# Performance work log

Measured on AMD Instinct MI355X. Metric: run time of the kernel, lower is better.

Reference implementation:

```python
import jax, jax.numpy as jnp
import numpy as np

TEMPERATURE = 0.5
EPS = 1e-8  # torch F.cosine_similarity norm clamp


def setup_inputs() -> dict:
    key = jax.random.key(0)
    k1, k2 = jax.random.split(key)
    B, D = 4096, 512
    return {
        "features_1": jax.random.normal(k1, (B, D), dtype=jnp.float32),
        "features_2": jax.random.normal(k2, (B, D), dtype=jnp.float32),
    }


def reference(features_1, features_2):
    B = features_1.shape[0]
    z = jnp.concatenate([features_1, features_2], axis=0)  # [2B, D]
    norm = jnp.maximum(jnp.linalg.norm(z, axis=1, keepdims=True), EPS)
    zn = z / norm
    # pairwise cosine similarity via single GEMM instead of (2B,2B,D) broadcast
    logits = (zn @ zn.T) / TEMPERATURE  # [2B, 2B]
    labels = jnp.concatenate([jnp.arange(B), jnp.arange(B)])  # [2B]
    logp = jax.nn.log_softmax(logits, axis=1)
    loss = -jnp.mean(logp[jnp.arange(2 * B), labels])
    return loss
```

## Files before the change

kernel.cpp:

```cpp
#include <hip/hip_runtime.h>
#include <hip/hip_bf16.h>

#define B_ROWS 4096
#define N2 8192
#define DD 512
#define NBLK 544

typedef __attribute__((ext_vector_type(4))) float float4v;
typedef __attribute__((ext_vector_type(2))) long long2v;

__global__ __launch_bounds__(256) void k_norm_tgt(const float* __restrict__ f1,
                                                  const float* __restrict__ f2,
                                                  unsigned char* __restrict__ zn8,
                                                  float* __restrict__ tpart,
                                                  float* __restrict__ rowsum) {
  int w = threadIdx.x >> 6, lane = threadIdx.x & 63;
  int j = blockIdx.x * 4 + w;
  const float4* s1 = (const float4*)(f1 + (size_t)j * DD);
  const float4* s2 = (const float4*)(f2 + (size_t)j * DD);
  float4 a0 = s1[lane * 2], a1 = s1[lane * 2 + 1];
  float4 b0 = s2[lane * 2], b1 = s2[lane * 2 + 1];
  float ss1 = a0.x * a0.x + a0.y * a0.y + a0.z * a0.z + a0.w * a0.w +
              a1.x * a1.x + a1.y * a1.y + a1.z * a1.z + a1.w * a1.w;
  float ss2 = b0.x * b0.x + b0.y * b0.y + b0.z * b0.z + b0.w * b0.w +
              b1.x * b1.x + b1.y * b1.y + b1.z * b1.z + b1.w * b1.w;
  float ab = a0.x * b0.x + a0.y * b0.y + a0.z * b0.z + a0.w * b0.w +
             a1.x * b1.x + a1.y * b1.y + a1.z * b1.z + a1.w * b1.w;
#pragma unroll
  for (int o = 1; o < 64; o <<= 1) {
    ss1 += __shfl_xor(ss1, o, 64);
    ss2 += __shfl_xor(ss2, o, 64);
    ab += __shfl_xor(ab, o, 64);
  }
  float inv1 = 1.0f / fmaxf(sqrtf(ss1), 1e-8f);
  float inv2 = 1.0f / fmaxf(sqrtf(ss2), 1e-8f);

  uint2 q;
  int lo = __builtin_amdgcn_cvt_pk_fp8_f32(a0.x * inv1, a0.y * inv1, 0, false);
  lo = __builtin_amdgcn_cvt_pk_fp8_f32(a0.z * inv1, a0.w * inv1, lo, true);
  q.x = (unsigned int)lo;
  lo = __builtin_amdgcn_cvt_pk_fp8_f32(a1.x * inv1, a1.y * inv1, 0, false);
  lo = __builtin_amdgcn_cvt_pk_fp8_f32(a1.z * inv1, a1.w * inv1, lo, true);
  q.y = (unsigned int)lo;
  ((uint2*)(zn8 + (size_t)j * DD))[lane] = q;

  lo = __builtin_amdgcn_cvt_pk_fp8_f32(b0.x * inv2, b0.y * inv2, 0, false);
  lo = __builtin_amdgcn_cvt_pk_fp8_f32(b0.z * inv2, b0.w * inv2, lo, true);
  q.x = (unsigned int)lo;
  lo = __builtin_amdgcn_cvt_pk_fp8_f32(b1.x * inv2, b1.y * inv2, 0, false);
  lo = __builtin_amdgcn_cvt_pk_fp8_f32(b1.z * inv2, b1.w * inv2, lo, true);
  q.y = (unsigned int)lo;
  ((uint2*)(zn8 + (size_t)(B_ROWS + j) * DD))[lane] = q;

  if (lane == 0) tpart[j] = 2.0f + 2.0f * ab * inv1 * inv2;
  if (threadIdx.x < 8) rowsum[blockIdx.x * 8 + threadIdx.x] = 0.f;
}

__global__ __launch_bounds__(256, 4) void k_gemm_expsum(const unsigned char* __restrict__ zn8,
                                                        float* __restrict__ rowsum) {
  __shared__ __align__(16) char bbuf[32768];
  __shared__ float colaccum[512];

  int g = blockIdx.x;

  int P = 0, off = 0;
  for (;;) {
    int nb = (128 - 2 * P + 7) >> 3;
    if (g < off + nb) break;
    off += nb;
    ++P;
  }
  int c = g - off;
  int j0 = 2 * P + 8 * c;
  int nt = 128 - j0; if (nt > 8) nt = 8;
  const int jmir0 = 2 * P + 2;

  const int tid = threadIdx.x;
  const int lane = tid & 63, w = tid >> 6;
  const int lr = lane & 15, hi2 = lane >> 4;
  const char* zb = (const char*)zn8;
  const int arow0 = P * 128;

  colaccum[tid] = 0.f;
  colaccum[tid + 256] = 0.f;

  int srow[8], scol[8];
#pragma unroll
  for (int cc = 0; cc < 8; ++cc) {
    int lo2 = cc * 4096 + tid * 16;
    srow[cc] = lo2 >> 9;
    scol[cc] = (lo2 & 511) ^ ((srow[cc] & 7) << 4);
  }

#define STAGE(rowbase) do {                                                              \
    _Pragma("unroll")                                                                    \
    for (int cc = 0; cc < 8; ++cc) {                                                     \
      const char* _s = zb + (size_t)((rowbase) + srow[cc]) * DD + scol[cc];              \
      __builtin_amdgcn_global_load_lds((__attribute__((address_space(1))) void*)_s,      \
          (__attribute__((address_space(3))) void*)(bbuf + cc * 4096 + tid * 16 - lane * 16), \
          16, 0, 0);                                                                     \
    }                                                                                    \
  } while (0)

  long2v aR[2][8];
  STAGE(arow0);
  __syncthreads();
  if (w < 2) {
#pragma unroll
    for (int m = 0; m < 2; ++m) {
      int rr = (w << 5) + (m << 4) + lr;
      const char* rowp = bbuf + rr * DD;
      int sz = (rr & 7) << 4;
#pragma unroll
      for (int p = 0; p < 8; ++p)
        aR[m][p] = *(const long2v*)(rowp + ((p * 64 + hi2 * 16) ^ sz));
    }
  }
  __syncthreads();
  STAGE(arow0 + 64);
  __syncthreads();
  if (w >= 2) {
#pragma unroll
    for (int m = 0; m < 2; ++m) {
      int rr = ((w - 2) << 5) + (m << 4) + lr;
      const char* rowp = bbuf + rr * DD;
      int sz = (rr & 7) << 4;
#pragma unroll
      for (int p = 0; p < 8; ++p)
        aR[m][p] = *(const long2v*)(rowp + ((p * 64 + hi2 * 16) ^ sz));
    }
  }
  __syncthreads();

  float rowacc[2][4];
#pragma unroll
  for (int m = 0; m < 2; ++m)
#pragma unroll
    for (int r = 0; r < 4; ++r) rowacc[m][r] = 0.f;

  const float Cc = 2.88539008177792681f;
  for (int t = 0; t < nt; ++t) {
    STAGE((j0 + t) * 64);
    __syncthreads();

    float4v acc[2][4];
#pragma unroll
    for (int m = 0; m < 2; ++m)
#pragma unroll
      for (int n = 0; n < 4; ++n) acc[m][n] = {0.f, 0.f, 0.f, 0.f};

#pragma unroll
    for (int n = 0; n < 4; ++n) {
      long2v bR[8];
      int col = (n << 4) + lr;
      const char* colp = bbuf + col * DD;
      int sz = (col & 7) << 4;
#pragma unroll
      for (int p = 0; p < 8; ++p)
        bR[p] = *(const long2v*)(colp + ((p * 64 + hi2 * 16) ^ sz));
#pragma unroll
      for (int p = 0; p < 8; ++p)
#pragma unroll
        for (int m = 0; m < 2; ++m) {
          acc[m][n] = __builtin_amdgcn_mfma_f32_16x16x32_fp8_fp8(aR[m][p][0], bR[p][0], acc[m][n], 0, 0, 0);
          acc[m][n] = __builtin_amdgcn_mfma_f32_16x16x32_fp8_fp8(aR[m][p][1], bR[p][1], acc[m][n], 0, 0, 0);
        }
    }

    float colp4[4] = {0.f, 0.f, 0.f, 0.f};
#pragma unroll
    for (int m = 0; m < 2; ++m)
#pragma unroll
      for (int n = 0; n < 4; ++n)
#pragma unroll
        for (int r = 0; r < 4; ++r) {
          float e = exp2f(fmaf(acc[m][n][r], Cc, -Cc));
          rowacc[m][r] += e;
          colp4[n] += e;
        }
    if ((j0 + t) >= jmir0) {
#pragma unroll
      for (int n = 0; n < 4; ++n) {
        float v = colp4[n];
        v += __shfl_xor(v, 16);
        v += __shfl_xor(v, 32);
        if (hi2 == 0) atomicAdd(&colaccum[(t << 6) + (n << 4) + lr], v);
      }
    }
    __syncthreads();
  }
#undef STAGE

#pragma unroll
  for (int m = 0; m < 2; ++m)
#pragma unroll
    for (int r = 0; r < 4; ++r) {
      float v = rowacc[m][r];
      v += __shfl_xor(v, 1);
      v += __shfl_xor(v, 2);
      v += __shfl_xor(v, 4);
      v += __shfl_xor(v, 8);
      if (lr == 0)
        atomicAdd(&rowsum[arow0 + (w << 5) + (m << 4) + (hi2 << 2) + r], v);
    }
  for (int idx = tid; idx < nt * 64; idx += 256) {
    float v = colaccum[idx];
    if (v != 0.f) atomicAdd(&rowsum[(j0 + (idx >> 6)) * 64 + (idx & 63)], v);
  }
}

__global__ __launch_bounds__(1024) void k_finalize(const float* __restrict__ rowsum,
                                                   const float* __restrict__ tpart,
                                                   float* __restrict__ out) {
  int t = threadIdx.x;
  float acc = 0.f;
  for (int i = t; i < N2; i += 1024) acc += 2.0f + logf(rowsum[i]);
  for (int i = t; i < B_ROWS; i += 1024) acc -= tpart[i];
#pragma unroll
  for (int o = 32; o; o >>= 1) acc += __shfl_down(acc, o, 64);
  __shared__ float wsum[16];
  if ((t & 63) == 0) wsum[t >> 6] = acc;
  __syncthreads();
  if (t == 0) {
    float s = 0.f;
#pragma unroll
    for (int k = 0; k < 16; ++k) s += wsum[k];
    out[0] = s * (1.0f / (float)N2);
  }
}

extern "C" void kernel_launch(void* const* d_in, const int* in_sizes, int n_in,
                              void* d_out, int out_size, void* d_ws, size_t ws_size,
                              hipStream_t stream) {
  const float* f1 = (const float*)d_in[0];
  const float* f2 = (const float*)d_in[1];
  float* out = (float*)d_out;
  char* ws = (char*)d_ws;

  unsigned char* zn8 = (unsigned char*)ws;
  float* rowsum = (float*)(ws + (size_t)N2 * DD);
  float* tpart = rowsum + N2;

  k_norm_tgt<<<B_ROWS / 4, 256, 0, stream>>>(f1, f2, zn8, tpart, rowsum);
  k_gemm_expsum<<<NBLK, 256, 0, stream>>>(zn8, rowsum);
  k_finalize<<<1, 1024, 0, stream>>>(rowsum, tpart, out);
}
```

Measured before the change: 70.10 us.

## Shrink GEMM row tile from 128 to 64 rows and double block count

Each block in the symmetric GEMM+exp-sum kernel now covers a 64-row A panel instead of 128, and each wave holds one 16-row fragment instead of two. The triangular tile schedule is recomputed for 64-row panels, so the grid doubles to 1088 blocks. This is meant to spread work more evenly across CUs and lower per-thread register use. In exchange, every B tile is reused by half as many A rows, so LDS staging traffic and column atomics roughly double. The column-sum flush also drops its zero check and skips the diagonal tile by index instead.

```diff
diff --git a/kernel.cpp b/kernel.cpp
--- a/kernel.cpp
+++ b/kernel.cpp
@@ -4,7 +4,7 @@
 #define B_ROWS 4096
 #define N2 8192
 #define DD 512
-#define NBLK 544
+#define NBLK 1088
 
 typedef __attribute__((ext_vector_type(4))) float float4v;
 typedef __attribute__((ext_vector_type(2))) long long2v;
@@ -65,21 +65,20 @@
 
   int P = 0, off = 0;
   for (;;) {
-    int nb = (128 - 2 * P + 7) >> 3;
+    int nb = (128 - P + 7) >> 3;
     if (g < off + nb) break;
     off += nb;
     ++P;
   }
   int c = g - off;
-  int j0 = 2 * P + 8 * c;
+  int j0 = P + 8 * c;
   int nt = 128 - j0; if (nt > 8) nt = 8;
-  const int jmir0 = 2 * P + 2;
 
   const int tid = threadIdx.x;
   const int lane = tid & 63, w = tid >> 6;
   const int lr = lane & 15, hi2 = lane >> 4;
   const char* zb = (const char*)zn8;
-  const int arow0 = P * 128;
+  const int arow0 = P * 64;
 
   colaccum[tid] = 0.f;
   colaccum[tid + 256] = 0.f;
@@ -97,57 +96,34 @@
     for (int cc = 0; cc < 8; ++cc) {                                                     \
       const char* _s = zb + (size_t)((rowbase) + srow[cc]) * DD + scol[cc];              \
       __builtin_amdgcn_global_load_lds((__attribute__((address_space(1))) void*)_s,      \
-          (__attribute__((address_space(3))) void*)(bbuf + cc * 4096 + tid * 16 - lane * 16), \
+          (__attribute__((address_space(3))) void*)(bbuf + cc * 4096 + (w << 10)),       \
           16, 0, 0);                                                                     \
     }                                                                                    \
   } while (0)
 
-  long2v aR[2][8];
+  long2v aR[8];
   STAGE(arow0);
   __syncthreads();
-  if (w < 2) {
-#pragma unroll
-    for (int m = 0; m < 2; ++m) {
-      int rr = (w << 5) + (m << 4) + lr;
-      const char* rowp = bbuf + rr * DD;
-      int sz = (rr & 7) << 4;
-#pragma unroll
-      for (int p = 0; p < 8; ++p)
-        aR[m][p] = *(const long2v*)(rowp + ((p * 64 + hi2 * 16) ^ sz));
-    }
+  {
+    int rr = (w << 4) + lr;
+    const char* rowp = bbuf + rr * DD;
+    int sz = (rr & 7) << 4;
+#pragma unroll
+    for (int p = 0; p < 8; ++p)
+      aR[p] = *(const long2v*)(rowp + ((p * 64 + hi2 * 16) ^ sz));
   }
   __syncthreads();
-  STAGE(arow0 + 64);
-  __syncthreads();
-  if (w >= 2) {
-#pragma unroll
-    for (int m = 0; m < 2; ++m) {
-      int rr = ((w - 2) << 5) + (m << 4) + lr;
-      const char* rowp = bbuf + rr * DD;
-      int sz = (rr & 7) << 4;
-#pragma unroll
-      for (int p = 0; p < 8; ++p)
-        aR[m][p] = *(const long2v*)(rowp + ((p * 64 + hi2 * 16) ^ sz));
-    }
-  }
-  __syncthreads();
-
-  float rowacc[2][4];
-#pragma unroll
-  for (int m = 0; m < 2; ++m)
-#pragma unroll
-    for (int r = 0; r < 4; ++r) rowacc[m][r] = 0.f;
-
+
+  float rowacc[4] = {0.f, 0.f, 0.f, 0.f};
   const float Cc = 2.88539008177792681f;
+
   for (int t = 0; t < nt; ++t) {
     STAGE((j0 + t) * 64);
     __syncthreads();
 
-    float4v acc[2][4];
-#pragma unroll
-    for (int m = 0; m < 2; ++m)
-#pragma unroll
-      for (int n = 0; n < 4; ++n) acc[m][n] = {0.f, 0.f, 0.f, 0.f};
+    float4v acc[4];
+#pragma unroll
+    for (int n = 0; n < 4; ++n) acc[n] = {0.f, 0.f, 0.f, 0.f};
 
 #pragma unroll
     for (int n = 0; n < 4; ++n) {
@@ -159,26 +135,22 @@
       for (int p = 0; p < 8; ++p)
         bR[p] = *(const long2v*)(colp + ((p * 64 + hi2 * 16) ^ sz));
 #pragma unroll
-      for (int p = 0; p < 8; ++p)
-#pragma unroll
-        for (int m = 0; m < 2; ++m) {
-          acc[m][n] = __builtin_amdgcn_mfma_f32_16x16x32_fp8_fp8(aR[m][p][0], bR[p][0], acc[m][n], 0, 0, 0);
-          acc[m][n] = __builtin_amdgcn_mfma_f32_16x16x32_fp8_fp8(aR[m][p][1], bR[p][1], acc[m][n], 0, 0, 0);
-        }
+      for (int p = 0; p < 8; ++p) {
+        acc[n] = __builtin_amdgcn_mfma_f32_16x16x32_fp8_fp8(aR[p][0], bR[p][0], acc[n], 0, 0, 0);
+        acc[n] = __builtin_amdgcn_mfma_f32_16x16x32_fp8_fp8(aR[p][1], bR[p][1], acc[n], 0, 0, 0);
+      }
     }
 
     float colp4[4] = {0.f, 0.f, 0.f, 0.f};
 #pragma unroll
-    for (int m = 0; m < 2; ++m)
-#pragma unroll
-      for (int n = 0; n < 4; ++n)
-#pragma unroll
-        for (int r = 0; r < 4; ++r) {
-          float e = exp2f(fmaf(acc[m][n][r], Cc, -Cc));
-          rowacc[m][r] += e;
-          colp4[n] += e;
-        }
-    if ((j0 + t) >= jmir0) {
+    for (int n = 0; n < 4; ++n)
+#pragma unroll
+      for (int r = 0; r < 4; ++r) {
+        float e = exp2f(fmaf(acc[n][r], Cc, -Cc));
+        rowacc[r] += e;
+        colp4[n] += e;
+      }
+    if ((j0 + t) > P) {
 #pragma unroll
       for (int n = 0; n < 4; ++n) {
         float v = colp4[n];
@@ -192,21 +164,17 @@
 #undef STAGE
 
 #pragma unroll
-  for (int m = 0; m < 2; ++m)
-#pragma unroll
-    for (int r = 0; r < 4; ++r) {
-      float v = rowacc[m][r];
-      v += __shfl_xor(v, 1);
-      v += __shfl_xor(v, 2);
-      v += __shfl_xor(v, 4);
-      v += __shfl_xor(v, 8);
-      if (lr == 0)
-        atomicAdd(&rowsum[arow0 + (w << 5) + (m << 4) + (hi2 << 2) + r], v);
-    }
-  for (int idx = tid; idx < nt * 64; idx += 256) {
-    float v = colaccum[idx];
-    if (v != 0.f) atomicAdd(&rowsum[(j0 + (idx >> 6)) * 64 + (idx & 63)], v);
-  }
+  for (int r = 0; r < 4; ++r) {
+    float v = rowacc[r];
+    v += __shfl_xor(v, 1);
+    v += __shfl_xor(v, 2);
+    v += __shfl_xor(v, 4);
+    v += __shfl_xor(v, 8);
+    if (lr == 0)
+      atomicAdd(&rowsum[arow0 + (w << 4) + (hi2 << 2) + r], v);
+  }
+  for (int idx = tid + (c == 0 ? 64 : 0); idx < nt * 64; idx += 256)
+    atomicAdd(&rowsum[(j0 + (idx >> 6)) * 64 + (idx & 63)], colaccum[idx]);
 }
 
 __global__ __launch_bounds__(1024) void k_finalize(const float* __restrict__ rowsum,
```

Measured after the change: 69.56 us. About the same (-0.8%).

## Load GEMM operands directly from global memory and halve tiles per block

Applied to the files above, without the earlier changes.

Removes the LDS staging buffer and its per-tile barriers, so the fp8 A and B fragments are read straight from global memory (L2) into registers. It also halves the number of column tiles per block from 8 to 4, roughly doubling the grid. The occupancy hint drops to 3 waves per SIMD. Removing the barriers and LDS traffic is meant to increase overlap, at the cost of uncoalesced 16-byte global reads per lane and more redundant A-tile loads across blocks.

```diff
diff --git a/kernel.cpp b/kernel.cpp
--- a/kernel.cpp
+++ b/kernel.cpp
@@ -4,7 +4,7 @@
 #define B_ROWS 4096
 #define N2 8192
 #define DD 512
-#define NBLK 544
+#define NBLK 1056
 
 typedef __attribute__((ext_vector_type(4))) float float4v;
 typedef __attribute__((ext_vector_type(2))) long long2v;
@@ -56,24 +56,22 @@
   if (threadIdx.x < 8) rowsum[blockIdx.x * 8 + threadIdx.x] = 0.f;
 }
 
-__global__ __launch_bounds__(256, 4) void k_gemm_expsum(const unsigned char* __restrict__ zn8,
+__global__ __launch_bounds__(256, 3) void k_gemm_expsum(const unsigned char* __restrict__ zn8,
                                                         float* __restrict__ rowsum) {
-  __shared__ __align__(16) char bbuf[32768];
-  __shared__ float colaccum[512];
+  __shared__ float colaccum[256];
 
   int g = blockIdx.x;
 
   int P = 0, off = 0;
   for (;;) {
-    int nb = (128 - 2 * P + 7) >> 3;
+    int nb = (131 - 2 * P) >> 2;
     if (g < off + nb) break;
     off += nb;
     ++P;
   }
   int c = g - off;
-  int j0 = 2 * P + 8 * c;
-  int nt = 128 - j0; if (nt > 8) nt = 8;
-  const int jmir0 = 2 * P + 2;
+  const int j0 = 2 * P + 4 * c;
+  int nt = 128 - j0; if (nt > 4) nt = 4;
 
   const int tid = threadIdx.x;
   const int lane = tid & 63, w = tid >> 6;
@@ -81,56 +79,17 @@
   const char* zb = (const char*)zn8;
   const int arow0 = P * 128;
 
-  colaccum[tid] = 0.f;
-  colaccum[tid + 256] = 0.f;
-
-  int srow[8], scol[8];
-#pragma unroll
-  for (int cc = 0; cc < 8; ++cc) {
-    int lo2 = cc * 4096 + tid * 16;
-    srow[cc] = lo2 >> 9;
-    scol[cc] = (lo2 & 511) ^ ((srow[cc] & 7) << 4);
-  }
-
-#define STAGE(rowbase) do {                                                              \
-    _Pragma("unroll")                                                                    \
-    for (int cc = 0; cc < 8; ++cc) {                                                     \
-      const char* _s = zb + (size_t)((rowbase) + srow[cc]) * DD + scol[cc];              \
-      __builtin_amdgcn_global_load_lds((__attribute__((address_space(1))) void*)_s,      \
-          (__attribute__((address_space(3))) void*)(bbuf + cc * 4096 + tid * 16 - lane * 16), \
-          16, 0, 0);                                                                     \
-    }                                                                                    \
-  } while (0)
+  if (tid < 256) colaccum[tid] = 0.f;
+  __syncthreads();
 
   long2v aR[2][8];
-  STAGE(arow0);
-  __syncthreads();
-  if (w < 2) {
-#pragma unroll
-    for (int m = 0; m < 2; ++m) {
-      int rr = (w << 5) + (m << 4) + lr;
-      const char* rowp = bbuf + rr * DD;
-      int sz = (rr & 7) << 4;
-#pragma unroll
-      for (int p = 0; p < 8; ++p)
-        aR[m][p] = *(const long2v*)(rowp + ((p * 64 + hi2 * 16) ^ sz));
-    }
-  }
-  __syncthreads();
-  STAGE(arow0 + 64);
-  __syncthreads();
-  if (w >= 2) {
-#pragma unroll
-    for (int m = 0; m < 2; ++m) {
-      int rr = ((w - 2) << 5) + (m << 4) + lr;
-      const char* rowp = bbuf + rr * DD;
-      int sz = (rr & 7) << 4;
-#pragma unroll
-      for (int p = 0; p < 8; ++p)
-        aR[m][p] = *(const long2v*)(rowp + ((p * 64 + hi2 * 16) ^ sz));
-    }
-  }
-  __syncthreads();
+#pragma unroll
+  for (int m = 0; m < 2; ++m) {
+    const char* rowp = zb + (size_t)(arow0 + (w << 5) + (m << 4) + lr) * DD + hi2 * 16;
+#pragma unroll
+    for (int p = 0; p < 8; ++p)
+      aR[m][p] = *(const long2v*)(rowp + p * 64);
+  }
 
   float rowacc[2][4];
 #pragma unroll
@@ -139,10 +98,9 @@
     for (int r = 0; r < 4; ++r) rowacc[m][r] = 0.f;
 
   const float Cc = 2.88539008177792681f;
+
   for (int t = 0; t < nt; ++t) {
-    STAGE((j0 + t) * 64);
-    __syncthreads();
-
+    const int jt = j0 + t;
     float4v acc[2][4];
 #pragma unroll
     for (int m = 0; m < 2; ++m)
@@ -152,12 +110,10 @@
 #pragma unroll
     for (int n = 0; n < 4; ++n) {
       long2v bR[8];
-      int col = (n << 4) + lr;
-      const char* colp = bbuf + col * DD;
-      int sz = (col & 7) << 4;
+      const char* colp = zb + (size_t)(jt * 64 + (n << 4) + lr) * DD + hi2 * 16;
 #pragma unroll
       for (int p = 0; p < 8; ++p)
-        bR[p] = *(const long2v*)(colp + ((p * 64 + hi2 * 16) ^ sz));
+        bR[p] = *(const long2v*)(colp + p * 64);
 #pragma unroll
       for (int p = 0; p < 8; ++p)
 #pragma unroll
@@ -178,7 +134,7 @@
           rowacc[m][r] += e;
           colp4[n] += e;
         }
-    if ((j0 + t) >= jmir0) {
+    if (jt >= 2 * P + 2) {
 #pragma unroll
       for (int n = 0; n < 4; ++n) {
         float v = colp4[n];
@@ -187,9 +143,7 @@
         if (hi2 == 0) atomicAdd(&colaccum[(t << 6) + (n << 4) + lr], v);
       }
     }
-    __syncthreads();
-  }
-#undef STAGE
+  }
 
 #pragma unroll
   for (int m = 0; m < 2; ++m)
@@ -203,10 +157,10 @@
       if (lr == 0)
         atomicAdd(&rowsum[arow0 + (w << 5) + (m << 4) + (hi2 << 2) + r], v);
     }
-  for (int idx = tid; idx < nt * 64; idx += 256) {
-    float v = colaccum[idx];
-    if (v != 0.f) atomicAdd(&rowsum[(j0 + (idx >> 6)) * 64 + (idx & 63)], v);
-  }
+
+  __syncthreads();
+  for (int idx = tid + (c == 0 ? 128 : 0); idx < nt * 64; idx += 256)
+    atomicAdd(&rowsum[(j0 + (idx >> 6)) * 64 + (idx & 63)], colaccum[idx]);
 }
 
 __global__ __launch_bounds__(1024) void k_finalize(const float* __restrict__ rowsum,
```

After: 113.9 us. +62.5%, slower.
